# Kernel tuning notes

Measured on AMD Instinct MI355X. Metric: run time of the kernel, lower is better.

The kernel has to match this reference:

```python
import jax, jax.numpy as jnp
import numpy as np

N_NODES = 100000
EPS = 1e-5


def gcn_conv(x, W, b, src, dst, n):
    # PyG GCNConv: linear transform first, then normalized propagation with self-loops
    x = x @ W  # [N, out]
    loop = jnp.arange(n)
    s = jnp.concatenate([src, loop])
    d = jnp.concatenate([dst, loop])
    deg = jax.ops.segment_sum(jnp.ones(s.shape, x.dtype), d, num_segments=n)
    dinv = jnp.where(deg > 0, jax.lax.rsqrt(deg), 0.0)
    norm = dinv[s] * dinv[d]  # [E+N]
    msg = x[s] * norm[:, None]  # gather from source
    out = jax.ops.segment_sum(msg, d, num_segments=n)  # scatter-add to target
    return out + b


def batch_norm(x, gamma, beta):
    mu = jnp.mean(x, axis=0)
    var = jnp.var(x, axis=0)
    return (x - mu) * jax.lax.rsqrt(var + EPS) * gamma + beta


def setup_inputs() -> dict:
    key = jax.random.key(0)
    ks = jax.random.split(key, 12)
    x = jax.random.normal(ks[0], (N_NODES, 128), dtype=jnp.float32)
    edge_index = jax.random.randint(ks[1], (2, 3200000), 0, N_NODES, dtype=jnp.int64)
    def lin(k, fin, fout):
        lim = 1.0 / np.sqrt(fin)
        return jax.random.uniform(k, (fin, fout), jnp.float32, -lim, lim)
    return {
        "x": x, "edge_index": edge_index,
        "W1": lin(ks[2], 128, 8), "b1": jnp.zeros(8), "g1": jnp.ones(8), "be1": jnp.zeros(8),
        "W2": lin(ks[3], 8, 16), "b2": jnp.zeros(16), "g2": jnp.ones(16), "be2": jnp.zeros(16),
        "W3": lin(ks[4], 16, 16), "b3": jnp.zeros(16), "g3": jnp.ones(16), "be3": jnp.zeros(16),
        "W4": lin(ks[5], 16, 8), "b4": jnp.zeros(8), "g4": jnp.ones(8), "be4": jnp.zeros(8),
        "Wout": lin(ks[6], 8, 1), "bout": jnp.zeros(1),
    }


def reference(x, edge_index, W1, b1, g1, be1, W2, b2, g2, be2, W3, b3, g3, be3, W4, b4, g4, be4, Wout, bout):
    src, dst = edge_index[0], edge_index[1]
    n = x.shape[0]
    h = jax.nn.relu(batch_norm(gcn_conv(x, W1, b1, src, dst, n), g1, be1))
    h = jax.nn.relu(batch_norm(gcn_conv(h, W2, b2, src, dst, n), g2, be2))
    h = jax.nn.relu(batch_norm(gcn_conv(h, W3, b3, src, dst, n), g3, be3))
    h = jax.nn.relu(batch_norm(gcn_conv(h, W4, b4, src, dst, n), g4, be4))
    pooled = jnp.max(h, axis=0, keepdims=True)  # global_max_pool with batch=None -> [1, 8]
    return (pooled @ Wout + bout).squeeze(1)  # [1]
```

## Files before the change

### kernel.cpp

```cpp
#include <hip/hip_runtime.h>
#include <hip/hip_fp16.h>
#include <cstddef>

#define EPS 1e-5f
#define TILE 4096

__global__ void k_init(float* __restrict__ stats, int* __restrict__ bhist) {
    int t = threadIdx.x;
    if (t < 256) stats[t] = 0.f;
    bhist[t] = 0;
}

__global__ void k_bhist(const int* __restrict__ dst, int* __restrict__ bhist,
                        int E, int nbk) {
    __shared__ int hist[512];
    int tid = threadIdx.x;
    int tile0 = blockIdx.x * TILE;
    for (int i = tid; i < nbk; i += 256) hist[i] = 0;
    __syncthreads();
    #pragma unroll
    for (int k = 0; k < 16; ++k) {
        int e = tile0 + k * 256 + tid;
        if (e < E) atomicAdd(&hist[dst[e] >> 8], 1);
    }
    __syncthreads();
    for (int i = tid; i < nbk; i += 256) {
        int c = hist[i];
        if (c) atomicAdd(&bhist[i], c);
    }
}

__global__ void k_bscan(const int* __restrict__ bhist, int* __restrict__ bcur,
                        int* __restrict__ bstart, int nbk, int E) {
    __shared__ int tmp[512];
    int t = threadIdx.x;
    int v = (t < nbk) ? bhist[t] : 0;
    tmp[t] = v;
    __syncthreads();
    for (int off = 1; off < 512; off <<= 1) {
        int y = (t >= off) ? tmp[t - off] : 0;
        __syncthreads();
        tmp[t] += y;
        __syncthreads();
    }
    if (t < nbk) { int ex = tmp[t] - v; bcur[t] = ex; bstart[t] = ex; }
    if (t == 0) bstart[nbk] = E;
}

__global__ void k_part(const int* __restrict__ src, const int* __restrict__ dst,
                       int* __restrict__ bcur, unsigned int* __restrict__ part,
                       int E, int nbk) {
    __shared__ int hist[512];
    __shared__ int base[512];
    int tid = threadIdx.x;
    int tile0 = blockIdx.x * TILE;
    for (int i = tid; i < nbk; i += 256) hist[i] = 0;
    __syncthreads();
    unsigned int rec[16];
    int bk[16];
    #pragma unroll
    for (int k = 0; k < 16; ++k) {
        int e = tile0 + k * 256 + tid;
        bk[k] = -1;
        if (e < E) {
            int d = dst[e], s = src[e];
            bk[k] = d >> 8;
            rec[k] = ((unsigned int)(d & 255) << 24) | (unsigned int)s;
            atomicAdd(&hist[bk[k]], 1);
        }
    }
    __syncthreads();
    for (int i = tid; i < nbk; i += 256) {
        int c = hist[i];
        base[i] = c ? atomicAdd(&bcur[i], c) : 0;
        hist[i] = 0;
    }
    __syncthreads();
    #pragma unroll
    for (int k = 0; k < 16; ++k) {
        if (bk[k] >= 0) {
            int r = atomicAdd(&hist[bk[k]], 1);
            part[base[bk[k]] + r] = rec[k];
        }
    }
}

__global__ void k_fill2(const unsigned int* __restrict__ part, const int* __restrict__ bstart,
                        float* __restrict__ dinv, int* __restrict__ row_start,
                        int* __restrict__ csr_src, int N) {
    __shared__ int hist[256];
    __shared__ int cur[256];
    __shared__ int wsum[8];
    int b = blockIdx.x, tid = threadIdx.x;
    int nbase = b << 8;
    int span0 = bstart[b], span1 = bstart[b + 1];
    if (tid < 256) hist[tid] = 0;
    __syncthreads();
    for (int i = span0 + tid; i < span1; i += 512)
        atomicAdd(&hist[part[i] >> 24], 1);
    __syncthreads();
    int v = (tid < 256) ? hist[tid] : 0;
    int lane = tid & 63, wid = tid >> 6;
    int x = v;
    #pragma unroll
    for (int off = 1; off < 64; off <<= 1) {
        int y = __shfl_up(x, off);
        if (lane >= off) x += y;
    }
    if (lane == 63) wsum[wid] = x;
    __syncthreads();
    int add = 0;
    for (int w = 0; w < wid && w < 4; ++w) add += wsum[w];
    int incl = x + add;
    int rs = span0 + incl - v;
    int node = nbase + tid;
    if (tid < 256 && node < N) {
        row_start[node] = rs;
        dinv[node] = rsqrtf((float)(v + 1));
        if (node == N - 1) row_start[N] = rs + v;
    }
    if (tid < 256) cur[tid] = rs;
    __syncthreads();
    for (int i = span0 + tid; i < span1; i += 512) {
        unsigned int rec = part[i];
        int p = atomicAdd(&cur[rec >> 24], 1);
        csr_src[p] = (int)(rec & 0xFFFFFFu);
    }
}

#define TN 64
__global__ void k_lin1(const float* __restrict__ x, const float* __restrict__ W,
                       const float* __restrict__ dinv,
                       __half* __restrict__ hs, int n) {
    __shared__ float xs[TN * 132];
    __shared__ float ws[128 * 8];
    int tid = threadIdx.x;
    int base = blockIdx.x * TN;
    for (int i = tid; i < 1024; i += 256) ws[i] = W[i];
    int nvalid = n - base; if (nvalid > TN) nvalid = TN;
    int limit4 = nvalid * 32;
    const float4* x4 = (const float4*)(x + (size_t)base * 128);
    float4* xs4 = (float4*)xs;
    for (int i = tid; i < TN * 32; i += 256) {
        if (i < limit4) {
            int row = i >> 5, col = i & 31;
            xs4[row * 33 + col] = x4[i];
        }
    }
    __syncthreads();
    #pragma unroll
    for (int rep = 0; rep < 2; ++rep) {
        int o = rep * 256 + tid;
        int node = o >> 3, feat = o & 7;
        if (node < nvalid) {
            const float* xr = xs + node * 132;
            float s = 0.f;
            #pragma unroll 8
            for (int k = 0; k < 128; ++k) s = fmaf(xr[k], ws[k * 8 + feat], s);
            s *= dinv[base + node];
            hs[(size_t)(base + node) * 8 + feat] = __float2half(s);
        }
    }
}

template<int F>
__global__ void k_gather(const int* __restrict__ row_start, const int* __restrict__ csr_src,
                         const float4* __restrict__ hp, const float* __restrict__ dinv,
                         float* __restrict__ acc, float* __restrict__ S, int n) {
    constexpr int P = F / 8;
    __shared__ float ls[2 * F];
    if (threadIdx.x < 2 * F) ls[threadIdx.x] = 0.f;
    __syncthreads();

    int t = blockIdx.x * blockDim.x + threadIdx.x;
    int node = (P == 1) ? t : (t >> 1);
    int part = (P == 1) ? 0 : (t & 1);

    float af[8];
    #pragma unroll
    for (int j = 0; j < 8; ++j) af[j] = 0.f;
    float di = 0.f;

    if (node < n) {
        {
            float4 r = hp[(size_t)node * P + part];
            const __half2* h = (const __half2*)&r;
            #pragma unroll
            for (int q = 0; q < 4; ++q) {
                float2 f = __half22float2(h[q]);
                af[2*q] += f.x; af[2*q+1] += f.y;
            }
        }
        int e = row_start[node], end = row_start[node + 1];
        for (; e + 1 < end; e += 2) {
            int s0 = csr_src[e], s1 = csr_src[e + 1];
            float4 r0 = hp[(size_t)s0 * P + part];
            float4 r1 = hp[(size_t)s1 * P + part];
            const __half2* h0 = (const __half2*)&r0;
            const __half2* h1 = (const __half2*)&r1;
            #pragma unroll
            for (int q = 0; q < 4; ++q) {
                float2 f0 = __half22float2(h0[q]);
                float2 f1 = __half22float2(h1[q]);
                af[2*q]   += f0.x + f1.x;
                af[2*q+1] += f0.y + f1.y;
            }
        }
        if (e < end) {
            int s0 = csr_src[e];
            float4 r0 = hp[(size_t)s0 * P + part];
            const __half2* h0 = (const __half2*)&r0;
            #pragma unroll
            for (int q = 0; q < 4; ++q) {
                float2 f0 = __half22float2(h0[q]);
                af[2*q] += f0.x; af[2*q+1] += f0.y;
            }
        }
        float4* ap = (float4*)(acc + (size_t)node * F + part * 8);
        float4 o0, o1;
        o0.x = af[0]; o0.y = af[1]; o0.z = af[2]; o0.w = af[3];
        o1.x = af[4]; o1.y = af[5]; o1.z = af[6]; o1.w = af[7];
        ap[0] = o0; ap[1] = o1;
        di = dinv[node];
    }

    float s1v[8], s2v[8];
    #pragma unroll
    for (int j = 0; j < 8; ++j) {
        float v = af[j] * di;
        s1v[j] = v; s2v[j] = v * v;
    }
    #pragma unroll
    for (int j = 0; j < 8; ++j) {
        #pragma unroll
        for (int off = P; off < 64; off <<= 1) {
            s1v[j] += __shfl_down(s1v[j], off);
            s2v[j] += __shfl_down(s2v[j], off);
        }
    }
    int lane = threadIdx.x & 63;
    if (lane < P) {
        int j0 = part * 8;
        #pragma unroll
        for (int j = 0; j < 8; ++j) {
            atomicAdd(&ls[j0 + j], s1v[j]);
            atomicAdd(&ls[F + j0 + j], s2v[j]);
        }
    }
    __syncthreads();
    if (threadIdx.x < 2 * F) atomicAdd(&S[threadIdx.x], ls[threadIdx.x]);
}

template<int FIN, int FOUT>
__global__ void k_bnlin(const float* __restrict__ acc, const float* __restrict__ dinv,
                        const float* __restrict__ S,
                        const float* __restrict__ g, const float* __restrict__ be,
                        const float* __restrict__ W,
                        __half* __restrict__ hs, int n) {
    __shared__ float sc[FIN], sh[FIN], ws[FIN * FOUT];
    int tid = threadIdx.x;
    if (tid < FIN) {
        float mu = S[tid] / (float)n;
        float var = S[FIN + tid] / (float)n - mu * mu;
        float inv = rsqrtf(var + EPS) * g[tid];
        sc[tid] = inv;
        sh[tid] = be[tid] - mu * inv;
    }
    for (int i = tid; i < FIN * FOUT; i += blockDim.x) ws[i] = W[i];
    __syncthreads();
    int i = blockIdx.x * blockDim.x + tid;
    if (i >= n) return;
    float di = dinv[i];
    float xr[FIN];
    const float4* ap = (const float4*)(acc + (size_t)i * FIN);
    #pragma unroll
    for (int q = 0; q < FIN / 4; ++q) {
        float4 a = ap[q];
        xr[4*q+0] = fmaxf(fmaf(a.x * di, sc[4*q+0], sh[4*q+0]), 0.f);
        xr[4*q+1] = fmaxf(fmaf(a.y * di, sc[4*q+1], sh[4*q+1]), 0.f);
        xr[4*q+2] = fmaxf(fmaf(a.z * di, sc[4*q+2], sh[4*q+2]), 0.f);
        xr[4*q+3] = fmaxf(fmaf(a.w * di, sc[4*q+3], sh[4*q+3]), 0.f);
    }
    float out[FOUT];
    #pragma unroll
    for (int j = 0; j < FOUT; ++j) {
        float s = 0.f;
        #pragma unroll
        for (int k = 0; k < FIN; ++k) s = fmaf(xr[k], ws[k * FOUT + j], s);
        out[j] = s * di;
    }
    float4 pk[FOUT / 8];
    __half2* ph = (__half2*)pk;
    #pragma unroll
    for (int j = 0; j < FOUT / 2; ++j)
        ph[j] = __floats2half2_rn(out[2*j], out[2*j+1]);
    float4* hp = (float4*)(hs + (size_t)i * FOUT);
    #pragma unroll
    for (int q = 0; q < FOUT / 8; ++q) hp[q] = pk[q];
}

__global__ void k_bnmax(const float* __restrict__ acc, const float* __restrict__ dinv,
                        const float* __restrict__ S,
                        const float* __restrict__ g, const float* __restrict__ be,
                        float* __restrict__ bmax, int n) {
    __shared__ float sc[8], sh[8];
    __shared__ float wmax[4 * 8];
    int tid = threadIdx.x;
    if (tid < 8) {
        float mu = S[tid] / (float)n;
        float var = S[8 + tid] / (float)n - mu * mu;
        float inv = rsqrtf(var + EPS) * g[tid];
        sc[tid] = inv;
        sh[tid] = be[tid] - mu * inv;
    }
    __syncthreads();
    int i = blockIdx.x * blockDim.x + tid;
    float vals[8];
    #pragma unroll
    for (int j = 0; j < 8; ++j) vals[j] = 0.f;
    if (i < n) {
        float di = dinv[i];
        const float4* ap = (const float4*)(acc + (size_t)i * 8);
        #pragma unroll
        for (int q = 0; q < 2; ++q) {
            float4 a = ap[q];
            vals[4*q+0] = fmaxf(fmaf(a.x * di, sc[4*q+0], sh[4*q+0]), 0.f);
            vals[4*q+1] = fmaxf(fmaf(a.y * di, sc[4*q+1], sh[4*q+1]), 0.f);
            vals[4*q+2] = fmaxf(fmaf(a.z * di, sc[4*q+2], sh[4*q+2]), 0.f);
            vals[4*q+3] = fmaxf(fmaf(a.w * di, sc[4*q+3], sh[4*q+3]), 0.f);
        }
    }
    #pragma unroll
    for (int j = 0; j < 8; ++j) {
        #pragma unroll
        for (int off = 32; off > 0; off >>= 1)
            vals[j] = fmaxf(vals[j], __shfl_down(vals[j], off));
    }
    int lane = tid & 63, wid = tid >> 6;
    if (lane == 0) {
        #pragma unroll
        for (int j = 0; j < 8; ++j) wmax[wid * 8 + j] = vals[j];
    }
    __syncthreads();
    if (tid < 8) {
        float m = wmax[tid];
        #pragma unroll
        for (int w = 1; w < 4; ++w) m = fmaxf(m, wmax[w * 8 + tid]);
        bmax[blockIdx.x * 8 + tid] = m;
    }
}

__global__ void k_final(const float* __restrict__ bmax, const float* __restrict__ Wout,
                        const float* __restrict__ bout, float* __restrict__ out, int nb) {
    __shared__ float red[64 * 8];
    int tid = threadIdx.x;
    int j = tid & 7, c = tid >> 3;
    float m = 0.f;
    for (int b = c; b < nb; b += 64) m = fmaxf(m, bmax[b * 8 + j]);
    red[c * 8 + j] = m;
    __syncthreads();
    if (tid < 8) {
        float mm = red[tid];
        for (int cc = 1; cc < 64; ++cc) mm = fmaxf(mm, red[cc * 8 + tid]);
        red[tid] = mm;
    }
    __syncthreads();
    if (tid == 0) {
        float s = bout[0];
        #pragma unroll
        for (int k = 0; k < 8; ++k) s = fmaf(red[k], Wout[k], s);
        out[0] = s;
    }
}

extern "C" void kernel_launch(void* const* d_in, const int* in_sizes, int n_in,
                              void* d_out, int out_size, void* d_ws, size_t ws_size,
                              hipStream_t stream) {
    const float* x    = (const float*)d_in[0];
    const int*   ei   = (const int*)d_in[1];
    const float* W1   = (const float*)d_in[2];
    const float* g1   = (const float*)d_in[4];
    const float* be1  = (const float*)d_in[5];
    const float* W2   = (const float*)d_in[6];
    const float* g2   = (const float*)d_in[8];
    const float* be2  = (const float*)d_in[9];
    const float* W3   = (const float*)d_in[10];
    const float* g3   = (const float*)d_in[12];
    const float* be3  = (const float*)d_in[13];
    const float* W4   = (const float*)d_in[14];
    const float* g4   = (const float*)d_in[16];
    const float* be4  = (const float*)d_in[17];
    const float* Wout = (const float*)d_in[18];
    const float* bout = (const float*)d_in[19];
    float* out = (float*)d_out;

    const int N = in_sizes[0] / 128;
    const int E = in_sizes[1] / 2;
    const int* src = ei;
    const int* dst = ei + E;
    const int nbk = (N + 255) >> 8;
    const int gT  = (E + TILE - 1) / TILE;

    char* ws = (char*)d_ws;
    size_t o = 0;
    float* dinv      = (float*)(ws + o); o += 4 * (size_t)N;
    int*   row_start = (int*)(ws + o);   o += 4 * ((size_t)N + 16);
    float* stats     = (float*)(ws + o); o += 4096;
    int*   bhist     = (int*)(ws + o);   o += 2048;
    int*   bcur      = (int*)(ws + o);   o += 2048;
    int*   bstart    = (int*)(ws + o);   o += 4096;
    float* bmax      = (float*)(ws + o); o += 4 * (size_t)(((N + 255) / 256) * 8 + 64);
    size_t hsacc = 96 * (size_t)N;
    if ((size_t)4 * E > hsacc) hsacc = (size_t)4 * E;
    __half* hs       = (__half*)(ws + o);
    float*  acc      = (float*)(ws + o + 32 * (size_t)N);
    unsigned int* part = (unsigned int*)(ws + o);
    o += hsacc;
    int*   csr_src   = (int*)(ws + o);   o += 4 * (size_t)E;

    const int B = 256;
    int gN  = (N + B - 1) / B;
    int gN2 = (2 * N + B - 1) / B;

    k_init<<<1, 512, 0, stream>>>(stats, bhist);
    k_bhist<<<gT, B, 0, stream>>>(dst, bhist, E, nbk);
    k_bscan<<<1, 512, 0, stream>>>(bhist, bcur, bstart, nbk, E);
    k_part<<<gT, B, 0, stream>>>(src, dst, bcur, part, E, nbk);
    k_fill2<<<nbk, 512, 0, stream>>>(part, bstart, dinv, row_start, csr_src, N);

    k_lin1<<<(N + TN - 1) / TN, B, 0, stream>>>(x, W1, dinv, hs, N);
    k_gather<8><<<gN, B, 0, stream>>>(row_start, csr_src, (const float4*)hs, dinv, acc, stats + 0, N);

    k_bnlin<8, 16><<<gN, B, 0, stream>>>(acc, dinv, stats + 0, g1, be1, W2, hs, N);
    k_gather<16><<<gN2, B, 0, stream>>>(row_start, csr_src, (const float4*)hs, dinv, acc, stats + 32, N);

    k_bnlin<16, 16><<<gN, B, 0, stream>>>(acc, dinv, stats + 32, g2, be2, W3, hs, N);
    k_gather<16><<<gN2, B, 0, stream>>>(row_start, csr_src, (const float4*)hs, dinv, acc, stats + 64, N);

    k_bnlin<16, 8><<<gN, B, 0, stream>>>(acc, dinv, stats + 64, g3, be3, W4, hs, N);
    k_gather<8><<<gN, B, 0, stream>>>(row_start, csr_src, (const float4*)hs, dinv, acc, stats + 96, N);

    k_bnmax<<<gN, B, 0, stream>>>(acc, dinv, stats + 96, g4, be4, bmax, N);
    k_final<<<1, 512, 0, stream>>>(bmax, Wout, bout, out, gN);
}
```

Measured before the change: 405.5 us.

## Split each node's edge gather across two threads and use nontemporal memory ops

The CSR gather kernel now gives each node (and feature part) two threads. Each thread walks alternate edges, and the partial sums are combined with a shuffle-xor before one thread writes the result. This doubles the threads in flight, exposing more parallelism and memory-level concurrency for the irregular per-node edge loops (about 32 edges per node). Index loads, accumulator stores and the follow-up accumulator reads use nontemporal hints to limit cache pollution. The costs are more threads per launch, an extra shuffle step, and reduction offsets that had to be adjusted to match the new lane layout.

```diff
diff --git a/kernel.cpp b/kernel.cpp
--- a/kernel.cpp
+++ b/kernel.cpp
@@ -4,6 +4,8 @@
 
 #define EPS 1e-5f
 #define TILE 4096
+
+typedef float nf4 __attribute__((ext_vector_type(4)));
 
 __global__ void k_init(float* __restrict__ stats, int* __restrict__ bhist) {
     int t = threadIdx.x;
@@ -168,13 +170,15 @@
                          const float4* __restrict__ hp, const float* __restrict__ dinv,
                          float* __restrict__ acc, float* __restrict__ S, int n) {
     constexpr int P = F / 8;
+    constexpr int LOGP = (P == 2) ? 1 : 0;
     __shared__ float ls[2 * F];
     if (threadIdx.x < 2 * F) ls[threadIdx.x] = 0.f;
     __syncthreads();
 
     int t = blockIdx.x * blockDim.x + threadIdx.x;
-    int node = (P == 1) ? t : (t >> 1);
-    int part = (P == 1) ? 0 : (t & 1);
+    int node = t >> (LOGP + 1);
+    int part = t & (P - 1);
+    int sub  = (t >> LOGP) & 1;
 
     float af[8];
     #pragma unroll
@@ -182,7 +186,7 @@
     float di = 0.f;
 
     if (node < n) {
-        {
+        if (sub == 0) {
             float4 r = hp[(size_t)node * P + part];
             const __half2* h = (const __half2*)&r;
             #pragma unroll
@@ -191,9 +195,10 @@
                 af[2*q] += f.x; af[2*q+1] += f.y;
             }
         }
-        int e = row_start[node], end = row_start[node + 1];
-        for (; e + 1 < end; e += 2) {
-            int s0 = csr_src[e], s1 = csr_src[e + 1];
+        int e = row_start[node] + sub, end = row_start[node + 1];
+        for (; e + 2 < end; e += 4) {
+            int s0 = __builtin_nontemporal_load(&csr_src[e]);
+            int s1 = __builtin_nontemporal_load(&csr_src[e + 2]);
             float4 r0 = hp[(size_t)s0 * P + part];
             float4 r1 = hp[(size_t)s1 * P + part];
             const __half2* h0 = (const __half2*)&r0;
@@ -207,7 +212,7 @@
             }
         }
         if (e < end) {
-            int s0 = csr_src[e];
+            int s0 = __builtin_nontemporal_load(&csr_src[e]);
             float4 r0 = hp[(size_t)s0 * P + part];
             const __half2* h0 = (const __half2*)&r0;
             #pragma unroll
@@ -216,12 +221,17 @@
                 af[2*q] += f0.x; af[2*q+1] += f0.y;
             }
         }
-        float4* ap = (float4*)(acc + (size_t)node * F + part * 8);
-        float4 o0, o1;
-        o0.x = af[0]; o0.y = af[1]; o0.z = af[2]; o0.w = af[3];
-        o1.x = af[4]; o1.y = af[5]; o1.z = af[6]; o1.w = af[7];
-        ap[0] = o0; ap[1] = o1;
-        di = dinv[node];
+        #pragma unroll
+        for (int j = 0; j < 8; ++j) af[j] += __shfl_xor(af[j], P);
+        if (sub == 0) {
+            nf4* ap = (nf4*)(acc + (size_t)node * F + part * 8);
+            nf4 o0, o1;
+            o0.x = af[0]; o0.y = af[1]; o0.z = af[2]; o0.w = af[3];
+            o1.x = af[4]; o1.y = af[5]; o1.z = af[6]; o1.w = af[7];
+            __builtin_nontemporal_store(o0, ap);
+            __builtin_nontemporal_store(o1, ap + 1);
+            di = dinv[node];
+        }
     }
 
     float s1v[8], s2v[8];
@@ -233,7 +243,7 @@
     #pragma unroll
     for (int j = 0; j < 8; ++j) {
         #pragma unroll
-        for (int off = P; off < 64; off <<= 1) {
+        for (int off = 2 * P; off < 64; off <<= 1) {
             s1v[j] += __shfl_down(s1v[j], off);
             s2v[j] += __shfl_down(s2v[j], off);
         }
@@ -272,10 +282,10 @@
     if (i >= n) return;
     float di = dinv[i];
     float xr[FIN];
-    const float4* ap = (const float4*)(acc + (size_t)i * FIN);
+    const nf4* ap = (const nf4*)(acc + (size_t)i * FIN);
     #pragma unroll
     for (int q = 0; q < FIN / 4; ++q) {
-        float4 a = ap[q];
+        nf4 a = __builtin_nontemporal_load(ap + q);
         xr[4*q+0] = fmaxf(fmaf(a.x * di, sc[4*q+0], sh[4*q+0]), 0.f);
         xr[4*q+1] = fmaxf(fmaf(a.y * di, sc[4*q+1], sh[4*q+1]), 0.f);
         xr[4*q+2] = fmaxf(fmaf(a.z * di, sc[4*q+2], sh[4*q+2]), 0.f);
@@ -320,10 +330,10 @@
     for (int j = 0; j < 8; ++j) vals[j] = 0.f;
     if (i < n) {
         float di = dinv[i];
-        const float4* ap = (const float4*)(acc + (size_t)i * 8);
+        const nf4* ap = (const nf4*)(acc + (size_t)i * 8);
         #pragma unroll
         for (int q = 0; q < 2; ++q) {
-            float4 a = ap[q];
+            nf4 a = __builtin_nontemporal_load(ap + q);
             vals[4*q+0] = fmaxf(fmaf(a.x * di, sc[4*q+0], sh[4*q+0]), 0.f);
             vals[4*q+1] = fmaxf(fmaf(a.y * di, sc[4*q+1], sh[4*q+1]), 0.f);
             vals[4*q+2] = fmaxf(fmaf(a.z * di, sc[4*q+2], sh[4*q+2]), 0.f);
@@ -421,6 +431,7 @@
     const int B = 256;
     int gN  = (N + B - 1) / B;
     int gN2 = (2 * N + B - 1) / B;
+    int gN4 = (4 * N + B - 1) / B;
 
     k_init<<<1, 512, 0, stream>>>(stats, bhist);
     k_bhist<<<gT, B, 0, stream>>>(dst, bhist, E, nbk);
@@ -429,16 +440,16 @@
     k_fill2<<<nbk, 512, 0, stream>>>(part, bstart, dinv, row_start, csr_src, N);
 
     k_lin1<<<(N + TN - 1) / TN, B, 0, stream>>>(x, W1, dinv, hs, N);
-    k_gather<8><<<gN, B, 0, stream>>>(row_start, csr_src, (const float4*)hs, dinv, acc, stats + 0, N);
+    k_gather<8><<<gN2, B, 0, stream>>>(row_start, csr_src, (const float4*)hs, dinv, acc, stats + 0, N);
 
     k_bnlin<8, 16><<<gN, B, 0, stream>>>(acc, dinv, stats + 0, g1, be1, W2, hs, N);
-    k_gather<16><<<gN2, B, 0, stream>>>(row_start, csr_src, (const float4*)hs, dinv, acc, stats + 32, N);
+    k_gather<16><<<gN4, B, 0, stream>>>(row_start, csr_src, (const float4*)hs, dinv, acc, stats + 32, N);
 
     k_bnlin<16, 16><<<gN, B, 0, stream>>>(acc, dinv, stats + 32, g2, be2, W3, hs, N);
-    k_gather<16><<<gN2, B, 0, stream>>>(row_start, csr_src, (const float4*)hs, dinv, acc, stats + 64, N);
+    k_gather<16><<<gN4, B, 0, stream>>>(row_start, csr_src, (const float4*)hs, dinv, acc, stats + 64, N);
 
     k_bnlin<16, 8><<<gN, B, 0, stream>>>(acc, dinv, stats + 64, g3, be3, W4, hs, N);
-    k_gather<8><<<gN, B, 0, stream>>>(row_start, csr_src, (const float4*)hs, dinv, acc, stats + 96, N);
+    k_gather<8><<<gN2, B, 0, stream>>>(row_start, csr_src, (const float4*)hs, dinv, acc, stats + 96, N);
 
     k_bnmax<<<gN, B, 0, stream>>>(acc, dinv, stats + 96, g4, be4, bmax, N);
     k_final<<<1, 512, 0, stream>>>(bmax, Wout, bout, out, gN);
```

Result: slower. 459.4 us (+13.3%).
